# Kernel tuning notes

Measured on AMD Instinct MI355X. Metric: run time of the kernel, lower is better.

The kernel has to match this reference:

```python
import jax, jax.numpy as jnp
import numpy as np
from jax import lax

B, N, C = 2, 4160, 512
HID = 2048
NUM_HEADS = 4
HEAD_DIM = C // NUM_HEADS
LN_EPS = 1e-5


def setup_inputs() -> dict:
    key = jax.random.key(0)
    ks = jax.random.split(key, 16)
    std = 0.02
    inp = {
        "x": jax.random.normal(ks[0], (B, N, C), dtype=jnp.float32),
        "ln1_w": jnp.ones((C,), jnp.float32), "ln1_b": jnp.zeros((C,), jnp.float32),
        "ln2_w": jnp.ones((C,), jnp.float32), "ln2_b": jnp.zeros((C,), jnp.float32),
        "q_w": jax.random.normal(ks[1], (C, C), jnp.float32) * std,
        "q_b": jnp.zeros((C,), jnp.float32),
        "kv_w": jax.random.normal(ks[2], (2 * C, C), jnp.float32) * std,
        "kv_b": jnp.zeros((2 * C,), jnp.float32),
        "proj_w": jax.random.normal(ks[3], (C, C), jnp.float32) * std,
        "proj_b": jnp.zeros((C,), jnp.float32),
        "fc1_w": jax.random.normal(ks[4], (HID, C), jnp.float32) * std,
        "fc1_b": jnp.zeros((HID,), jnp.float32),
        "dw_w": jax.random.normal(ks[5], (HID, 1, 3), jnp.float32) * np.sqrt(2.0 / 3.0),
        "dw_b": jnp.zeros((HID,), jnp.float32),
        "fc2_w": jax.random.normal(ks[6], (C, HID), jnp.float32) * std,
        "fc2_b": jnp.zeros((C,), jnp.float32),
        "px1_w": jax.random.normal(ks[7], (2 * C, C), jnp.float32) * std,
        "px1_b": jnp.zeros((2 * C,), jnp.float32),
        "px2_w": jax.random.normal(ks[8], (C, 2 * C), jnp.float32) * std,
        "px2_b": jnp.zeros((C,), jnp.float32),
        "gamma1": jnp.full((C,), 1e-6, jnp.float32),
        "gamma2": jnp.full((C,), 1e-6, jnp.float32),
        "H": 4096,
        "semantic_len": 64,
    }
    return inp


def _ln(x, w, b):
    mu = jnp.mean(x, axis=-1, keepdims=True)
    var = jnp.mean(jnp.square(x - mu), axis=-1, keepdims=True)
    return (x - mu) * lax.rsqrt(var + LN_EPS) * w + b


def _linear(x, w, b):
    return jnp.einsum('...i,oi->...o', x, w) + b


def _attention(x, q_w, q_b, kv_w, kv_b, proj_w, proj_b):
    b, n, c = x.shape
    h, d = NUM_HEADS, HEAD_DIM
    q = _linear(x, q_w, q_b).reshape(b, n, h, d).transpose(0, 2, 1, 3)   # bhnd
    kv = _linear(x, kv_w, kv_b).reshape(b, n, 2, h, d).transpose(2, 0, 3, 1, 4)
    k, v = kv[0], kv[1]                                                   # bhnd
    scale = d ** -0.5
    attn = jax.nn.softmax(jnp.einsum('bhnd,bhmd->bhnm', q, k) * scale, axis=-1)
    out = jnp.einsum('bhnm,bhmd->bhnd', attn, v).transpose(0, 2, 1, 3).reshape(b, n, c)
    return _linear(out, proj_w, proj_b)


def _dwconv(x, w, b):
    # x: [B, H, HID] -> conv over token axis, depthwise
    xt = x.transpose(0, 2, 1)  # NCH
    y = lax.conv_general_dilated(xt, w, window_strides=(1,), padding=((1, 1),),
                                 feature_group_count=HID,
                                 dimension_numbers=('NCH', 'OIH', 'NCH'))
    return (y + b[None, :, None]).transpose(0, 2, 1)


def _merge_ffn(x, H, fc1_w, fc1_b, dw_w, dw_b, fc2_w, fc2_b, px1_w, px1_b, px2_w, px2_b):
    seq = x[:, :H, :]
    sem = x[:, H:, :]
    sem = _linear(jax.nn.gelu(_linear(sem, px1_w, px1_b), approximate=False), px2_w, px2_b)
    seq = _linear(seq, fc1_w, fc1_b)
    seq = jax.nn.gelu(_dwconv(seq, dw_w, dw_b), approximate=False)
    seq = _linear(seq, fc2_w, fc2_b)
    return jnp.concatenate([seq, sem], axis=1)


def reference(x, ln1_w, ln1_b, ln2_w, ln2_b, q_w, q_b, kv_w, kv_b, proj_w, proj_b,
              fc1_w, fc1_b, dw_w, dw_b, fc2_w, fc2_b, px1_w, px1_b, px2_w, px2_b,
              gamma1, gamma2, H, semantic_len):
    x = x + gamma1 * _attention(_ln(x, ln1_w, ln1_b), q_w, q_b, kv_w, kv_b, proj_w, proj_b)
    x = x + gamma2 * _merge_ffn(_ln(x, ln2_w, ln2_b), H,
                                fc1_w, fc1_b, dw_w, dw_b, fc2_w, fc2_b,
                                px1_w, px1_b, px2_w, px2_b)
    return x
```

## Files before the change

kernel.cpp:

```cpp
#include <hip/hip_runtime.h>
#include <stdint.h>

#define BB 2
#define NN 4160
#define CC 512
#define HIDD 2048
#define HH 4096
#define QSCALE 0.12751742f
#define KSPLIT 6
#define KTILES 11

typedef short bf16x8 __attribute__((ext_vector_type(8)));
typedef float f32x4 __attribute__((ext_vector_type(4)));
typedef float f32x16 __attribute__((ext_vector_type(16)));

__device__ __forceinline__ float bf2f(ushort u){
  union { uint32_t u32; float f; } c; c.u32 = ((uint32_t)u) << 16; return c.f;
}
__device__ __forceinline__ ushort f2bf(float f){
  union { float f; uint32_t u32; } c; c.f = f;
  uint32_t r = c.u32 + 0x7fffu + ((c.u32 >> 16) & 1u);
  return (ushort)(r >> 16);
}
__device__ __forceinline__ float gelu_f(float x){
  return 0.5f * x * (1.0f + erff(x * 0.70710678118654752440f));
}
__device__ __forceinline__ void async16(ushort* lds, const ushort* g){
  __builtin_amdgcn_global_load_lds(
      (const __attribute__((address_space(1))) uint32_t*)g,
      (__attribute__((address_space(3))) uint32_t*)lds, 16, 0, 0);
}
__device__ __forceinline__ uint32_t cvtpk_bf16(float a, float b){
  uint32_t r;
  asm("v_cvt_pk_bf16_f32 %0, %1, %2" : "=v"(r) : "v"(a), "v"(b));
  return r;
}
__device__ __forceinline__ void swap32(uint32_t& x, uint32_t& y){
  asm("v_permlane32_swap_b32 %0, %1" : "+v"(x), "+v"(y));
}

template<int MODE>
__device__ __forceinline__ int rowmap(int m){
  if (MODE == 0) return m;
  if (MODE == 1) return (m >> 12) * NN + (m & 4095);
  return (m >> 6) * NN + HH + (m & 63);
}

__global__ __launch_bounds__(256) void wconv_kernel(
    const float* __restrict__ s0, const float* __restrict__ s1,
    const float* __restrict__ s2, const float* __restrict__ s3,
    const float* __restrict__ s4, const float* __restrict__ s5,
    const float* __restrict__ s6, ushort* __restrict__ dst)
{
  int i4 = (blockIdx.x * 256 + threadIdx.x) * 4;
  const float* s; int off;
  if      (i4 <  262144){ s = s0; off = 0;       }
  else if (i4 <  786432){ s = s1; off = 262144;  }
  else if (i4 < 1048576){ s = s2; off = 786432;  }
  else if (i4 < 2097152){ s = s3; off = 1048576; }
  else if (i4 < 3145728){ s = s4; off = 2097152; }
  else if (i4 < 3670016){ s = s5; off = 3145728; }
  else                  { s = s6; off = 3670016; }
  float4 v = *(const float4*)(s + (i4 - off));
  union { ushort h[4]; uint2 u; } o;
  o.h[0] = f2bf(v.x); o.h[1] = f2bf(v.y); o.h[2] = f2bf(v.z); o.h[3] = f2bf(v.w);
  *(uint2*)(dst + i4) = o.u;
}

__global__ __launch_bounds__(256) void ln_kernel(
    const float* __restrict__ x, const float* __restrict__ w,
    const float* __restrict__ b, ushort* __restrict__ out)
{
  int row  = blockIdx.x * 4 + (threadIdx.x >> 6);
  int lane = threadIdx.x & 63;
  const float4* xr = (const float4*)(x + (size_t)row * CC);
  float4 v0 = xr[lane];
  float4 v1 = xr[lane + 64];
  float s  = v0.x + v0.y + v0.z + v0.w + v1.x + v1.y + v1.z + v1.w;
  float ss = v0.x*v0.x + v0.y*v0.y + v0.z*v0.z + v0.w*v0.w
           + v1.x*v1.x + v1.y*v1.y + v1.z*v1.z + v1.w*v1.w;
  #pragma unroll
  for (int off = 1; off < 64; off <<= 1){
    s  += __shfl_xor(s, off);
    ss += __shfl_xor(ss, off);
  }
  float mu  = s * (1.0f / CC);
  float var = ss * (1.0f / CC) - mu * mu;
  float rs  = rsqrtf(var + 1e-5f);
  const float4* wp = (const float4*)w;
  const float4* bp = (const float4*)b;
  float4 w0 = wp[lane], w1 = wp[lane + 64], b0 = bp[lane], b1 = bp[lane + 64];
  union { ushort h[4]; uint2 u; } o0, o1;
  o0.h[0] = f2bf((v0.x - mu) * rs * w0.x + b0.x);
  o0.h[1] = f2bf((v0.y - mu) * rs * w0.y + b0.y);
  o0.h[2] = f2bf((v0.z - mu) * rs * w0.z + b0.z);
  o0.h[3] = f2bf((v0.w - mu) * rs * w0.w + b0.w);
  o1.h[0] = f2bf((v1.x - mu) * rs * w1.x + b1.x);
  o1.h[1] = f2bf((v1.y - mu) * rs * w1.y + b1.y);
  o1.h[2] = f2bf((v1.z - mu) * rs * w1.z + b1.z);
  o1.h[3] = f2bf((v1.w - mu) * rs * w1.w + b1.w);
  ushort* orow = out + (size_t)row * CC;
  ((uint2*)orow)[lane]      = o0.u;
  ((uint2*)orow)[lane + 64] = o1.u;
}

template<int BN, int AMAP, int OMAP, int EPI>
__global__ __launch_bounds__(256) void gemm_kernel(
    const ushort* __restrict__ A, int lda,
    const ushort* __restrict__ W,
    const float* __restrict__ bias, const float* __restrict__ bias2,
    ushort* __restrict__ outb, ushort* __restrict__ outb2,
    float* __restrict__ outf,
    const float* __restrict__ resid, const float* __restrict__ gamma,
    ushort* __restrict__ vt, int K, int O)
{
  constexpr int NCT = BN / 32;
  __shared__ __align__(16) ushort As[2][128 * 64];
  __shared__ __align__(16) ushort Ws[2][BN * 64];
  int tid  = threadIdx.x;
  int lane = tid & 63;
  int wv   = tid >> 6;
  int w0   = wv & 1, w1 = wv >> 1;
  int quad = lane >> 4, l16 = lane & 15;
  int m0 = blockIdx.x * 128;
  int o0 = blockIdx.y * BN;

  auto stage = [&](int bsel, int k0){
    #pragma unroll
    for (int i = 0; i < 4; i++){
      int o = i * 256 + tid;
      int row = o >> 3, c = (o & 7) ^ (row & 7);
      int gm = rowmap<AMAP>(m0 + row);
      async16(&As[bsel][o * 8], A + (size_t)gm * lda + k0 + c * 8);
    }
    #pragma unroll
    for (int i = 0; i < BN * 8 / 256; i++){
      int o = i * 256 + tid;
      int row = o >> 3, c = (o & 7) ^ (row & 7);
      async16(&Ws[bsel][o * 8], W + (size_t)(o0 + row) * K + k0 + c * 8);
    }
  };

  f32x4 acc[4][NCT];
  f32x4 zf = {0.f, 0.f, 0.f, 0.f};
  #pragma unroll
  for (int i = 0; i < 4; i++)
    #pragma unroll
    for (int j = 0; j < NCT; j++) acc[i][j] = zf;

  stage(0, 0);
  int cur = 0;
  for (int k0 = 0; k0 < K; k0 += 64){
    __syncthreads();
    if (k0 + 64 < K) stage(cur ^ 1, k0 + 64);
    #pragma unroll
    for (int kk = 0; kk < 2; kk++){
      bf16x8 af[4], bfr[NCT];
      #pragma unroll
      for (int rt = 0; rt < 4; rt++){
        int row = w1 * 64 + rt * 16 + l16;
        af[rt] = *(const bf16x8*)&As[cur][(row * 8 + ((kk * 4 + quad) ^ (row & 7))) * 8];
      }
      #pragma unroll
      for (int ct = 0; ct < NCT; ct++){
        int row = w0 * (BN / 2) + ct * 16 + l16;
        bfr[ct] = *(const bf16x8*)&Ws[cur][(row * 8 + ((kk * 4 + quad) ^ (row & 7))) * 8];
      }
      #pragma unroll
      for (int rt = 0; rt < 4; rt++)
        #pragma unroll
        for (int ct = 0; ct < NCT; ct++)
          acc[rt][ct] = __builtin_amdgcn_mfma_f32_16x16x32_bf16(af[rt], bfr[ct], acc[rt][ct], 0, 0, 0);
    }
    cur ^= 1;
  }

  #pragma unroll
  for (int ct = 0; ct < NCT; ct++){
    int col = o0 + w0 * (BN / 2) + ct * 16 + l16;
    #pragma unroll
    for (int rt = 0; rt < 4; rt++){
      int mb = m0 + w1 * 64 + rt * 16 + quad * 4;
      if (EPI == 3){
        if (col < 512){
          float bs = bias[col];
          #pragma unroll
          for (int r = 0; r < 4; r++)
            outb[(size_t)(mb + r) * 512 + col] = f2bf((acc[rt][ct][r] + bs) * QSCALE);
        } else if (col < 1024){
          float bs = bias2[col - 512];
          #pragma unroll
          for (int r = 0; r < 4; r++)
            outb2[(size_t)(mb + r) * 512 + (col - 512)] = f2bf(acc[rt][ct][r] + bs);
        } else {
          float bs = bias2[col - 512];
          int dd = col - 1024;
          int h2 = dd >> 7, d = dd & 127;
          int bbat = (mb >= NN) ? 1 : 0;
          int n = mb - bbat * NN;
          union { ushort h[4]; uint2 u; } pk;
          #pragma unroll
          for (int r = 0; r < 4; r++) pk.h[r] = f2bf(acc[rt][ct][r] + bs);
          *(uint2*)&vt[((size_t)((bbat * 4 + h2) * 128 + d)) * NN + n] = pk.u;
        }
      } else {
        float bs = bias[col];
        #pragma unroll
        for (int r = 0; r < 4; r++){
          float v = acc[rt][ct][r] + bs;
          if (EPI == 1) v = gelu_f(v);
          if (EPI == 0 || EPI == 1){
            outb[(size_t)rowmap<OMAP>(mb + r) * O + col] = f2bf(v);
          } else {
            size_t off = (size_t)rowmap<OMAP>(mb + r) * O + col;
            outf[off] = resid[off] + gamma[col] * v;
          }
        }
      }
    }
  }
}

__global__ __launch_bounds__(256, 2) void attn_kernel(
    const ushort* __restrict__ q, const ushort* __restrict__ kbuf,
    const ushort* __restrict__ vt, ushort* __restrict__ opart, float* __restrict__ ml)
{
  __shared__ __align__(16) ushort Ks[2][64 * 128];
  __shared__ __align__(16) ushort VTs[2][128 * 64];
  __shared__ float Als[4][32];
  int tid = threadIdx.x, lane = tid & 63, wv = tid >> 6;
  int l31 = lane & 31, hf = lane >> 5;
  int qt = blockIdx.x, bh = blockIdx.y, ks = blockIdx.z;
  int b = bh >> 2, h = bh & 3;
  int jt0 = ks * KTILES;
  int jt1 = jt0 + KTILES; if (jt1 > 65) jt1 = 65;

  const ushort* kg0 = kbuf + ((size_t)b * NN) * CC + h * 128;
  const ushort* vg0 = vt + ((size_t)bh * 128) * NN;

  auto stage = [&](int bsel, int t){
    const ushort* kgb = kg0 + (size_t)(t * 64) * CC;
    const ushort* vgb = vg0 + t * 64;
    #pragma unroll
    for (int i = 0; i < 4; i++){
      int oo = i * 256 + tid;
      int row = oo >> 4, ck = (oo & 15) ^ (row & 7);
      async16(&Ks[bsel][oo * 8], kgb + (size_t)row * CC + ck * 8);
      int d = oo >> 3, cv = (oo & 7) ^ (d & 7);
      async16(&VTs[bsel][oo * 8], vgb + (size_t)d * NN + cv * 8);
    }
  };

  stage(0, jt0);

  int qr = qt * 128 + wv * 32 + l31;
  qr = (qr < NN) ? qr : (NN - 1);
  const ushort* qrow = q + ((size_t)(b * NN + qr)) * CC + h * 128 + hf * 8;
  bf16x8 qf[8];
  #pragma unroll
  for (int kk = 0; kk < 8; kk++)
    qf[kk] = *(const bf16x8*)(qrow + kk * 16);

  float mrow = -1e30f, lrow = 0.f;
  f32x16 o[4];
  #pragma unroll
  for (int dt = 0; dt < 4; dt++)
    #pragma unroll
    for (int r = 0; r < 16; r++) o[dt][r] = 0.f;

  int cur = 0;
  for (int jt = jt0; jt < jt1; jt++){
    __syncthreads();
    if (jt + 1 < jt1) stage(cur ^ 1, jt + 1);
    const ushort* Kb = Ks[cur];
    const ushort* Vb = VTs[cur];

    f32x16 s0, s1;
    #pragma unroll
    for (int r = 0; r < 16; r++){ s0[r] = 0.f; s1[r] = 0.f; }
    __builtin_amdgcn_s_setprio(1);
    #pragma unroll
    for (int kk = 0; kk < 8; kk++){
      int r0 = l31, r1 = 32 + l31;
      bf16x8 kf0 = *(const bf16x8*)&Kb[(r0 * 16 + ((kk * 2 + hf) ^ (r0 & 7))) * 8];
      bf16x8 kf1 = *(const bf16x8*)&Kb[(r1 * 16 + ((kk * 2 + hf) ^ (r1 & 7))) * 8];
      s0 = __builtin_amdgcn_mfma_f32_32x32x16_bf16(kf0, qf[kk], s0, 0, 0, 0);
      s1 = __builtin_amdgcn_mfma_f32_32x32x16_bf16(kf1, qf[kk], s1, 0, 0, 0);
    }
    __builtin_amdgcn_s_setprio(0);

    float mx = s0[0];
    #pragma unroll
    for (int r = 1; r < 16; r++) mx = fmaxf(mx, s0[r]);
    #pragma unroll
    for (int r = 0; r < 16; r++) mx = fmaxf(mx, s1[r]);
    mx = fmaxf(mx, __shfl_xor(mx, 32));

    if (__any(mx > mrow + 8.0f)){
      float mn = fmaxf(mrow, mx);
      float al = __builtin_amdgcn_exp2f(mrow - mn);
      mrow = mn;
      lrow *= al;
      if (lane < 32) Als[wv][l31] = al;
      #pragma unroll
      for (int g = 0; g < 4; g++){
        float4 ag = *(const float4*)&Als[wv][8 * g + 4 * hf];
        float agr[4] = {ag.x, ag.y, ag.z, ag.w};
        #pragma unroll
        for (int dt = 0; dt < 4; dt++)
          #pragma unroll
          for (int r = 0; r < 4; r++)
            o[dt][4 * g + r] *= agr[r];
      }
    }

    float t = 0.f;
    #pragma unroll
    for (int r = 0; r < 16; r++){ s0[r] = __builtin_amdgcn_exp2f(s0[r] - mrow); t += s0[r]; }
    #pragma unroll
    for (int r = 0; r < 16; r++){ s1[r] = __builtin_amdgcn_exp2f(s1[r] - mrow); t += s1[r]; }
    t += __shfl_xor(t, 32);
    lrow += t;

    union PU { uint32_t w[4]; bf16x8 v; };
    bf16x8 pa[4];
    {
      uint32_t Aw = cvtpk_bf16(s0[0],  s0[1]);
      uint32_t Bw = cvtpk_bf16(s0[2],  s0[3]);
      uint32_t Cw = cvtpk_bf16(s0[4],  s0[5]);
      uint32_t Dw = cvtpk_bf16(s0[6],  s0[7]);
      swap32(Aw, Cw); swap32(Bw, Dw);
      PU u0; u0.w[0] = Aw; u0.w[1] = Bw; u0.w[2] = Cw; u0.w[3] = Dw; pa[0] = u0.v;
      uint32_t Ew = cvtpk_bf16(s0[8],  s0[9]);
      uint32_t Fw = cvtpk_bf16(s0[10], s0[11]);
      uint32_t Gw = cvtpk_bf16(s0[12], s0[13]);
      uint32_t Hw = cvtpk_bf16(s0[14], s0[15]);
      swap32(Ew, Gw); swap32(Fw, Hw);
      PU u1; u1.w[0] = Ew; u1.w[1] = Fw; u1.w[2] = Gw; u1.w[3] = Hw; pa[1] = u1.v;
      uint32_t Iw = cvtpk_bf16(s1[0],  s1[1]);
      uint32_t Jw = cvtpk_bf16(s1[2],  s1[3]);
      uint32_t Kw = cvtpk_bf16(s1[4],  s1[5]);
      uint32_t Lw = cvtpk_bf16(s1[6],  s1[7]);
      swap32(Iw, Kw); swap32(Jw, Lw);
      PU u2; u2.w[0] = Iw; u2.w[1] = Jw; u2.w[2] = Kw; u2.w[3] = Lw; pa[2] = u2.v;
      uint32_t Mw = cvtpk_bf16(s1[8],  s1[9]);
      uint32_t Nw = cvtpk_bf16(s1[10], s1[11]);
      uint32_t Ow = cvtpk_bf16(s1[12], s1[13]);
      uint32_t Pw = cvtpk_bf16(s1[14], s1[15]);
      swap32(Mw, Ow); swap32(Nw, Pw);
      PU u3; u3.w[0] = Mw; u3.w[1] = Nw; u3.w[2] = Ow; u3.w[3] = Pw; pa[3] = u3.v;
    }

    __builtin_amdgcn_s_setprio(1);
    #pragma unroll
    for (int k4 = 0; k4 < 4; k4++)
      #pragma unroll
      for (int dt = 0; dt < 4; dt++){
        int d = dt * 32 + l31;
        bf16x8 vf = *(const bf16x8*)&Vb[(d * 8 + ((k4 * 2 + hf) ^ (d & 7))) * 8];
        o[dt] = __builtin_amdgcn_mfma_f32_32x32x16_bf16(pa[k4], vf, o[dt], 0, 0, 0);
      }
    __builtin_amdgcn_s_setprio(0);
    cur ^= 1;
  }

  int part = (qt * 8 + bh) * KSPLIT + ks;
  if (lane < 32){
    ml[(size_t)part * 256 + wv * 32 + l31]       = mrow;
    ml[(size_t)part * 256 + 128 + wv * 32 + l31] = lrow;
  }
  ushort* op = opart + (size_t)part * 16384;
  #pragma unroll
  for (int g = 0; g < 4; g++)
    #pragma unroll
    for (int dt = 0; dt < 4; dt++){
      uint2 pk;
      pk.x = cvtpk_bf16(o[dt][4 * g + 0], o[dt][4 * g + 1]);
      pk.y = cvtpk_bf16(o[dt][4 * g + 2], o[dt][4 * g + 3]);
      *(uint2*)&op[((((wv * 4 + g) * 4 + dt) * 64) + lane) * 4] = pk;
    }
}

__global__ __launch_bounds__(256) void attn_combine_kernel(
    const ushort* __restrict__ opart, const float* __restrict__ ml,
    ushort* __restrict__ out)
{
  int qt = blockIdx.x, bh = blockIdx.y;
  int b = bh >> 2, hd = bh & 3;
  int tid = threadIdx.x, lane = tid & 63, wq = tid >> 6;
  int l31 = lane & 31, hf = lane >> 5;
  int base = (qt * 8 + bh) * KSPLIT;

  #pragma unroll
  for (int g = 0; g < 4; g++){
    int qb = wq * 32 + 8 * g + 4 * hf;
    float mv[KSPLIT][4], lv[KSPLIT][4];
    #pragma unroll
    for (int p = 0; p < KSPLIT; p++){
      float4 m = *(const float4*)&ml[(size_t)(base + p) * 256 + qb];
      float4 l = *(const float4*)&ml[(size_t)(base + p) * 256 + 128 + qb];
      mv[p][0] = m.x; mv[p][1] = m.y; mv[p][2] = m.z; mv[p][3] = m.w;
      lv[p][0] = l.x; lv[p][1] = l.y; lv[p][2] = l.z; lv[p][3] = l.w;
    }
    float wr[KSPLIT][4], invr[4];
    #pragma unroll
    for (int r = 0; r < 4; r++){
      float mx = mv[0][r];
      #pragma unroll
      for (int p = 1; p < KSPLIT; p++) mx = fmaxf(mx, mv[p][r]);
      float den = 0.f;
      #pragma unroll
      for (int p = 0; p < KSPLIT; p++){
        wr[p][r] = __builtin_amdgcn_exp2f(mv[p][r] - mx);
        den += wr[p][r] * lv[p][r];
      }
      invr[r] = 1.0f / den;
    }
    #pragma unroll
    for (int dt = 0; dt < 4; dt++){
      int idx = (((wq * 4 + g) * 4 + dt) * 64 + lane) * 4;
      float acc[4] = {0.f, 0.f, 0.f, 0.f};
      #pragma unroll
      for (int p = 0; p < KSPLIT; p++){
        union { ushort h[4]; uint2 u; } a;
        a.u = *(const uint2*)&opart[(size_t)(base + p) * 16384 + idx];
        #pragma unroll
        for (int r = 0; r < 4; r++) acc[r] += wr[p][r] * bf2f(a.h[r]);
      }
      #pragma unroll
      for (int r = 0; r < 4; r++){
        int n = qt * 128 + qb + r;
        if (n < NN)
          out[((size_t)(b * NN + n)) * CC + hd * 128 + dt * 32 + l31] = f2bf(acc[r] * invr[r]);
      }
    }
  }
}

__global__ __launch_bounds__(256) void dwconv_kernel(
    const ushort* __restrict__ u, const float* __restrict__ w,
    const float* __restrict__ bia, ushort* __restrict__ out)
{
  int g = blockIdx.x * 256 + threadIdx.x;
  int row = g >> 8;
  int c8 = (g & 255) * 8;
  int n = row & (HH - 1);
  size_t base = (size_t)row * HIDD + c8;
  uint4 z4; z4.x = z4.y = z4.z = z4.w = 0;
  uint4 u1 = *(const uint4*)(u + base);
  uint4 u0 = (n > 0)      ? *(const uint4*)(u + base - HIDD) : z4;
  uint4 u2 = (n < HH - 1) ? *(const uint4*)(u + base + HIDD) : z4;
  const ushort* p0 = (const ushort*)&u0;
  const ushort* p1 = (const ushort*)&u1;
  const ushort* p2 = (const ushort*)&u2;
  union { ushort h[8]; uint4 v; } o;
  #pragma unroll
  for (int k = 0; k < 8; k++){
    int c = c8 + k;
    float acc = bia[c] + w[c * 3] * bf2f(p0[k]) + w[c * 3 + 1] * bf2f(p1[k]) + w[c * 3 + 2] * bf2f(p2[k]);
    o.h[k] = f2bf(gelu_f(acc));
  }
  *(uint4*)(out + base) = o.v;
}

extern "C" void kernel_launch(void* const* d_in, const int* in_sizes, int n_in,
                              void* d_out, int out_size, void* d_ws, size_t ws_size,
                              hipStream_t stream)
{
  const float* x      = (const float*)d_in[0];
  const float* ln1w   = (const float*)d_in[1];
  const float* ln1b   = (const float*)d_in[2];
  const float* ln2w   = (const float*)d_in[3];
  const float* ln2b   = (const float*)d_in[4];
  const float* q_b    = (const float*)d_in[6];
  const float* kv_b   = (const float*)d_in[8];
  const float* proj_b = (const float*)d_in[10];
  const float* fc1_b  = (const float*)d_in[12];
  const float* dw_w   = (const float*)d_in[13];
  const float* dw_b   = (const float*)d_in[14];
  const float* fc2_b  = (const float*)d_in[16];
  const float* px1_b  = (const float*)d_in[18];
  const float* px2_b  = (const float*)d_in[20];
  const float* gamma1 = (const float*)d_in[21];
  const float* gamma2 = (const float*)d_in[22];
  float* out = (float*)d_out;

  char* ws = (char*)d_ws;
  ushort* wbf = (ushort*)(ws);
  ushort* lnb = (ushort*)(ws + 8388608);
  ushort* qb  = (ushort*)(ws + 16908288);
  ushort* kb  = (ushort*)(ws + 25427968);
  ushort* vtb = (ushort*)(ws + 33947648);
  ushort* ab  = (ushort*)(ws + 42467328);
  ushort* opart = (ushort*)(ws + 50987008);
  float*  mlb   = (float*)(ws + 102891520);
  ushort* f1  = (ushort*)(ws + 50987008);
  ushort* dg  = (ushort*)(ws + 84541440);
  ushort* sm1 = (ushort*)(ws + 118095872);

  ushort* wq    = wbf;
  ushort* wproj = wbf + 786432;
  ushort* wfc1  = wbf + 1048576;
  ushort* wfc2  = wbf + 2097152;
  ushort* wpx1  = wbf + 3145728;
  ushort* wpx2  = wbf + 3670016;

  wconv_kernel<<<4096, 256, 0, stream>>>((const float*)d_in[5], (const float*)d_in[7],
                                         (const float*)d_in[9], (const float*)d_in[11],
                                         (const float*)d_in[15], (const float*)d_in[17],
                                         (const float*)d_in[19], wbf);
  ln_kernel<<<2080, 256, 0, stream>>>(x, ln1w, ln1b, lnb);
  gemm_kernel<128,0,0,3><<<dim3(65, 12), 256, 0, stream>>>(
      lnb, 512, wq, q_b, kv_b, qb, kb, nullptr, nullptr, nullptr, vtb, 512, 1536);
  attn_kernel<<<dim3(33, 8, KSPLIT), 256, 0, stream>>>(qb, kb, vtb, opart, mlb);
  attn_combine_kernel<<<dim3(33, 8), 256, 0, stream>>>(opart, mlb, ab);
  gemm_kernel<64,0,0,2><<<dim3(65, 8), 256, 0, stream>>>(
      ab, 512, wproj, proj_b, nullptr, nullptr, nullptr, out, x, gamma1, nullptr, 512, 512);
  ln_kernel<<<2080, 256, 0, stream>>>(out, ln2w, ln2b, lnb);
  gemm_kernel<128,1,0,0><<<dim3(64, 16), 256, 0, stream>>>(
      lnb, 512, wfc1, fc1_b, nullptr, f1, nullptr, nullptr, nullptr, nullptr, nullptr, 512, 2048);
  dwconv_kernel<<<8192, 256, 0, stream>>>(f1, dw_w, dw_b, dg);
  gemm_kernel<64,0,1,2><<<dim3(64, 8), 256, 0, stream>>>(
      dg, 2048, wfc2, fc2_b, nullptr, nullptr, nullptr, out, out, gamma2, nullptr, 2048, 512);
  gemm_kernel<64,2,0,1><<<dim3(1, 16), 256, 0, stream>>>(
      lnb, 512, wpx1, px1_b, nullptr, sm1, nullptr, nullptr, nullptr, nullptr, nullptr, 512, 1024);
  gemm_kernel<64,0,2,2><<<dim3(1, 8), 256, 0, stream>>>(
      sm1, 1024, wpx2, px2_b, nullptr, nullptr, nullptr, out, out, gamma2, nullptr, 1024, 512);
}
```

Measured before the change: 456.2 us.

## Single-buffer V tile through registers to raise attention occupancy

```diff
diff --git a/kernel.cpp b/kernel.cpp
--- a/kernel.cpp
+++ b/kernel.cpp
@@ -221,12 +221,12 @@
   }
 }
 
-__global__ __launch_bounds__(256, 2) void attn_kernel(
+__global__ __launch_bounds__(256, 3) void attn_kernel(
     const ushort* __restrict__ q, const ushort* __restrict__ kbuf,
     const ushort* __restrict__ vt, ushort* __restrict__ opart, float* __restrict__ ml)
 {
   __shared__ __align__(16) ushort Ks[2][64 * 128];
-  __shared__ __align__(16) ushort VTs[2][128 * 64];
+  __shared__ __align__(16) ushort VTs[128 * 64];
   __shared__ float Als[4][32];
   int tid = threadIdx.x, lane = tid & 63, wv = tid >> 6;
   int l31 = lane & 31, hf = lane >> 5;
@@ -238,20 +238,28 @@
   const ushort* kg0 = kbuf + ((size_t)b * NN) * CC + h * 128;
   const ushort* vg0 = vt + ((size_t)bh * 128) * NN;
 
-  auto stage = [&](int bsel, int t){
+  auto stageK = [&](int bsel, int t){
     const ushort* kgb = kg0 + (size_t)(t * 64) * CC;
-    const ushort* vgb = vg0 + t * 64;
     #pragma unroll
     for (int i = 0; i < 4; i++){
       int oo = i * 256 + tid;
       int row = oo >> 4, ck = (oo & 15) ^ (row & 7);
       async16(&Ks[bsel][oo * 8], kgb + (size_t)row * CC + ck * 8);
+    }
+  };
+  uint4 vreg[4];
+  auto loadV = [&](int t){
+    const ushort* vgb = vg0 + t * 64;
+    #pragma unroll
+    for (int i = 0; i < 4; i++){
+      int oo = i * 256 + tid;
       int d = oo >> 3, cv = (oo & 7) ^ (d & 7);
-      async16(&VTs[bsel][oo * 8], vgb + (size_t)d * NN + cv * 8);
+      vreg[i] = *(const uint4*)(vgb + (size_t)d * NN + cv * 8);
     }
   };
 
-  stage(0, jt0);
+  stageK(0, jt0);
+  loadV(jt0);
 
   int qr = qt * 128 + wv * 32 + l31;
   qr = (qr < NN) ? qr : (NN - 1);
@@ -271,9 +279,14 @@
   int cur = 0;
   for (int jt = jt0; jt < jt1; jt++){
     __syncthreads();
-    if (jt + 1 < jt1) stage(cur ^ 1, jt + 1);
+    if (jt + 1 < jt1) stageK(cur ^ 1, jt + 1);
+    #pragma unroll
+    for (int i = 0; i < 4; i++){
+      int oo = i * 256 + tid;
+      *(uint4*)&VTs[oo * 8] = vreg[i];
+    }
+    if (jt + 1 < jt1) loadV(jt + 1);
     const ushort* Kb = Ks[cur];
-    const ushort* Vb = VTs[cur];
 
     f32x16 s0, s1;
     #pragma unroll
@@ -351,13 +364,17 @@
       PU u3; u3.w[0] = Mw; u3.w[1] = Nw; u3.w[2] = Ow; u3.w[3] = Pw; pa[3] = u3.v;
     }
 
+    asm volatile("s_waitcnt lgkmcnt(0)" ::: "memory");
+    __builtin_amdgcn_s_barrier();
+    __builtin_amdgcn_sched_barrier(0);
+
     __builtin_amdgcn_s_setprio(1);
     #pragma unroll
     for (int k4 = 0; k4 < 4; k4++)
       #pragma unroll
       for (int dt = 0; dt < 4; dt++){
         int d = dt * 32 + l31;
-        bf16x8 vf = *(const bf16x8*)&Vb[(d * 8 + ((k4 * 2 + hf) ^ (d & 7))) * 8];
+        bf16x8 vf = *(const bf16x8*)&VTs[(d * 8 + ((k4 * 2 + hf) ^ (d & 7))) * 8];
         o[dt] = __builtin_amdgcn_mfma_f32_32x32x16_bf16(pa[k4], vf, o[dt], 0, 0, 0);
       }
     __builtin_amdgcn_s_setprio(0);
```

Result: slower. 742.9 us (+62.8%).

## Merge semantic-token GEMMs into the FFN GEMM launches and reduce attention K-split

Applied to the files above, without the earlier changes.

```diff
diff --git a/kernel.cpp b/kernel.cpp
--- a/kernel.cpp
+++ b/kernel.cpp
@@ -7,8 +7,8 @@
 #define HIDD 2048
 #define HH 4096
 #define QSCALE 0.12751742f
-#define KSPLIT 6
-#define KTILES 11
+#define KSPLIT 4
+#define KTILES 17
 
 typedef short bf16x8 __attribute__((ext_vector_type(8)));
 typedef float f32x4 __attribute__((ext_vector_type(4)));
@@ -105,39 +105,38 @@
 }
 
 template<int BN, int AMAP, int OMAP, int EPI>
-__global__ __launch_bounds__(256) void gemm_kernel(
+__device__ __forceinline__ void gemm_body(
+    ushort* AsB, ushort* WsB,
     const ushort* __restrict__ A, int lda,
     const ushort* __restrict__ W,
     const float* __restrict__ bias, const float* __restrict__ bias2,
     ushort* __restrict__ outb, ushort* __restrict__ outb2,
     float* __restrict__ outf,
     const float* __restrict__ resid, const float* __restrict__ gamma,
-    ushort* __restrict__ vt, int K, int O)
+    ushort* __restrict__ vt, int K, int O, int m0, int o0)
 {
   constexpr int NCT = BN / 32;
-  __shared__ __align__(16) ushort As[2][128 * 64];
-  __shared__ __align__(16) ushort Ws[2][BN * 64];
   int tid  = threadIdx.x;
   int lane = tid & 63;
   int wv   = tid >> 6;
   int w0   = wv & 1, w1 = wv >> 1;
   int quad = lane >> 4, l16 = lane & 15;
-  int m0 = blockIdx.x * 128;
-  int o0 = blockIdx.y * BN;
 
   auto stage = [&](int bsel, int k0){
+    ushort* Asb = AsB + bsel * (128 * 64);
+    ushort* Wsb = WsB + bsel * (BN * 64);
     #pragma unroll
     for (int i = 0; i < 4; i++){
       int o = i * 256 + tid;
       int row = o >> 3, c = (o & 7) ^ (row & 7);
       int gm = rowmap<AMAP>(m0 + row);
-      async16(&As[bsel][o * 8], A + (size_t)gm * lda + k0 + c * 8);
+      async16(&Asb[o * 8], A + (size_t)gm * lda + k0 + c * 8);
     }
     #pragma unroll
     for (int i = 0; i < BN * 8 / 256; i++){
       int o = i * 256 + tid;
       int row = o >> 3, c = (o & 7) ^ (row & 7);
-      async16(&Ws[bsel][o * 8], W + (size_t)(o0 + row) * K + k0 + c * 8);
+      async16(&Wsb[o * 8], W + (size_t)(o0 + row) * K + k0 + c * 8);
     }
   };
 
@@ -153,18 +152,20 @@
   for (int k0 = 0; k0 < K; k0 += 64){
     __syncthreads();
     if (k0 + 64 < K) stage(cur ^ 1, k0 + 64);
+    const ushort* Asb = AsB + cur * (128 * 64);
+    const ushort* Wsb = WsB + cur * (BN * 64);
     #pragma unroll
     for (int kk = 0; kk < 2; kk++){
       bf16x8 af[4], bfr[NCT];
       #pragma unroll
       for (int rt = 0; rt < 4; rt++){
         int row = w1 * 64 + rt * 16 + l16;
-        af[rt] = *(const bf16x8*)&As[cur][(row * 8 + ((kk * 4 + quad) ^ (row & 7))) * 8];
+        af[rt] = *(const bf16x8*)&Asb[(row * 8 + ((kk * 4 + quad) ^ (row & 7))) * 8];
       }
       #pragma unroll
       for (int ct = 0; ct < NCT; ct++){
         int row = w0 * (BN / 2) + ct * 16 + l16;
-        bfr[ct] = *(const bf16x8*)&Ws[cur][(row * 8 + ((kk * 4 + quad) ^ (row & 7))) * 8];
+        bfr[ct] = *(const bf16x8*)&Wsb[(row * 8 + ((kk * 4 + quad) ^ (row & 7))) * 8];
       }
       #pragma unroll
       for (int rt = 0; rt < 4; rt++)
@@ -221,6 +222,48 @@
   }
 }
 
+template<int BN, int AMAP, int OMAP, int EPI>
+__global__ __launch_bounds__(256) void gemm_kernel(
+    const ushort* __restrict__ A, int lda,
+    const ushort* __restrict__ W,
+    const float* __restrict__ bias, const float* __restrict__ bias2,
+    ushort* __restrict__ outb, ushort* __restrict__ outb2,
+    float* __restrict__ outf,
+    const float* __restrict__ resid, const float* __restrict__ gamma,
+    ushort* __restrict__ vt, int K, int O)
+{
+  __shared__ __align__(16) ushort As[2][128 * 64];
+  __shared__ __align__(16) ushort Ws[2][BN * 64];
+  gemm_body<BN, AMAP, OMAP, EPI>(&As[0][0], &Ws[0][0],
+      A, lda, W, bias, bias2, outb, outb2, outf, resid, gamma, vt, K, O,
+      blockIdx.x * 128, blockIdx.y * BN);
+}
+
+template<int BN, int A0, int O0, int E0, int A1, int O1, int E1>
+__global__ __launch_bounds__(256) void gemm_dual(
+    const ushort* __restrict__ A, int lda,
+    const ushort* __restrict__ W, const float* __restrict__ bias,
+    ushort* __restrict__ outb, float* __restrict__ outf,
+    const float* __restrict__ resid, const float* __restrict__ gamma,
+    int K, int O, int gxm,
+    const ushort* __restrict__ Aa, int ldaa,
+    const ushort* __restrict__ Wa, const float* __restrict__ biasa,
+    ushort* __restrict__ outba, int Ka, int Oa, int gya)
+{
+  __shared__ __align__(16) ushort As[2][128 * 64];
+  __shared__ __align__(16) ushort Ws[2][BN * 64];
+  if ((int)blockIdx.x < gxm){
+    gemm_body<BN, A0, O0, E0>(&As[0][0], &Ws[0][0],
+        A, lda, W, bias, nullptr, outb, nullptr, outf, resid, gamma, nullptr,
+        K, O, blockIdx.x * 128, blockIdx.y * BN);
+  } else {
+    if ((int)blockIdx.y >= gya) return;
+    gemm_body<BN, A1, O1, E1>(&As[0][0], &Ws[0][0],
+        Aa, ldaa, Wa, biasa, nullptr, outba, nullptr, outf, resid, gamma, nullptr,
+        Ka, Oa, 0, blockIdx.y * BN);
+  }
+}
+
 __global__ __launch_bounds__(256, 2) void attn_kernel(
     const ushort* __restrict__ q, const ushort* __restrict__ kbuf,
     const ushort* __restrict__ vt, ushort* __restrict__ opart, float* __restrict__ ml)
@@ -493,7 +536,7 @@
   ushort* vtb = (ushort*)(ws + 33947648);
   ushort* ab  = (ushort*)(ws + 42467328);
   ushort* opart = (ushort*)(ws + 50987008);
-  float*  mlb   = (float*)(ws + 102891520);
+  float*  mlb   = (float*)(ws + 85590016);
   ushort* f1  = (ushort*)(ws + 50987008);
   ushort* dg  = (ushort*)(ws + 84541440);
   ushort* sm1 = (ushort*)(ws + 118095872);
@@ -517,13 +560,11 @@
   gemm_kernel<64,0,0,2><<<dim3(65, 8), 256, 0, stream>>>(
       ab, 512, wproj, proj_b, nullptr, nullptr, nullptr, out, x, gamma1, nullptr, 512, 512);
   ln_kernel<<<2080, 256, 0, stream>>>(out, ln2w, ln2b, lnb);
-  gemm_kernel<128,1,0,0><<<dim3(64, 16), 256, 0, stream>>>(
-      lnb, 512, wfc1, fc1_b, nullptr, f1, nullptr, nullptr, nullptr, nullptr, nullptr, 512, 2048);
+  gemm_dual<128, 1,0,0, 2,0,1><<<dim3(65, 16), 256, 0, stream>>>(
+      lnb, 512, wfc1, fc1_b, f1, nullptr, nullptr, nullptr, 512, 2048, 64,
+      lnb, 512, wpx1, px1_b, sm1, 512, 1024, 8);
   dwconv_kernel<<<8192, 256, 0, stream>>>(f1, dw_w, dw_b, dg);
-  gemm_kernel<64,0,1,2><<<dim3(64, 8), 256, 0, stream>>>(
-      dg, 2048, wfc2, fc2_b, nullptr, nullptr, nullptr, out, out, gamma2, nullptr, 2048, 512);
-  gemm_kernel<64,2,0,1><<<dim3(1, 16), 256, 0, stream>>>(
-      lnb, 512, wpx1, px1_b, nullptr, sm1, nullptr, nullptr, nullptr, nullptr, nullptr, 512, 1024);
-  gemm_kernel<64,0,2,2><<<dim3(1, 8), 256, 0, stream>>>(
-      sm1, 1024, wpx2, px2_b, nullptr, nullptr, nullptr, out, out, gamma2, nullptr, 1024, 512);
-}
+  gemm_dual<64, 0,1,2, 0,2,2><<<dim3(65, 8), 256, 0, stream>>>(
+      dg, 2048, wfc2, fc2_b, nullptr, out, out, gamma2, 2048, 512, 64,
+      sm1, 1024, wpx2, px2_b, nullptr, 1024, 512, 8);
+}
```

Result: no change. 464.6 us (+1.8%).
